# Kernel tuning notes

Hardware: AMD Instinct MI355X
Metric: run time of the kernel (lower is better)

The kernel has to match this reference:

```python
import jax, jax.numpy as jnp
import numpy as np

# ---- constants reconstructing the DMC lookup tables (topology_to_triangles, x/y/z, inner) ----
GRID = 32            # cells per axis -> offset grid is (GRID+1)^3
T = 48               # number of triangle-bearing topologies
MAXTRI = 4           # max triangles per topology (marching cubes)
EPS = 1e-8

# 12 marching-cubes edges of a cell: (corner offset dx,dy,dz, axis of edge)
EDGES = [(0,0,0,0),(1,0,0,1),(0,1,0,0),(0,0,0,1),
         (0,0,1,0),(1,0,1,1),(0,1,1,0),(0,0,1,1),
         (0,0,0,2),(1,0,0,2),(1,1,0,2),(0,1,0,2)]

# Deterministic stand-in for the MC triangle table: per topology, up to 4 triangles,
# each triangle = 3 edge indices in [0,12). TRI_MASK marks valid triangles.
_rs = np.random.RandomState(0)
TRI_TABLE = jnp.asarray(_rs.randint(0, 12, (T, MAXTRI, 3)))          # [T,4,3] int
_ntri = _rs.randint(1, MAXTRI + 1, (T,))
TRI_MASK = jnp.asarray((np.arange(MAXTRI)[None, :] < _ntri[:, None]).astype(np.float32))  # [T,4]


def _edge_vertices(offset):
    """offset: [3, G, G, G] -> per-cell edge vertex positions [N_cells, 12, 3].
    Vertex on an edge = edge midpoint + scalar offset along the edge axis."""
    ci = jnp.arange(GRID)
    I, J, K = jnp.meshgrid(ci, ci, ci, indexing='ij')  # [32,32,32]
    verts = []
    for (dx, dy, dz, a) in EDGES:  # fixed small loop over 12 edges
        gi, gj, gk = I + dx, J + dy, K + dz
        base = jnp.stack([gi, gj, gk], axis=-1).astype(offset.dtype)  # [32,32,32,3]
        disp = offset[a, gi, gj, gk]                                   # [32,32,32]
        unit = jnp.zeros((3,), offset.dtype).at[a].set(1.0)
        verts.append(base + (0.5 + disp)[..., None] * unit)
    V = jnp.stack(verts, axis=3)          # [32,32,32,12,3]
    return V.reshape(-1, 12, 3)            # [N,12,3]


def setup_inputs() -> dict:
    key = jax.random.key(0)
    k0, k1 = jax.random.split(key)
    offset = jax.random.normal(k0, (3, GRID + 1, GRID + 1, GRID + 1), dtype=jnp.float32)
    topology = jax.random.uniform(k1, (GRID ** 3, T), dtype=jnp.float32)
    return {"offset": offset, "topology": topology}


def reference(offset, topology):
    V = _edge_vertices(offset)                  # [N,12,3]
    tv = V[:, TRI_TABLE]                        # [N,T,4,3verts,3]  (irregular gather)
    # unnormalized face normals, then normalize
    n = jnp.cross(tv[..., 1, :] - tv[..., 0, :], tv[..., 2, :] - tv[..., 0, :])  # [N,T,4,3]
    n = n / (jnp.linalg.norm(n, axis=-1, keepdims=True) + EPS)

    # within-cell curvature: squared normal difference of consecutive triangle pairs
    d = n[:, :, 1:, :] - n[:, :, :-1, :]        # [N,T,3,3]
    pair_mask = TRI_MASK[:, 1:] * TRI_MASK[:, :-1]  # [T,3]
    within = jnp.einsum('ntpc,tp->nt', d * d, pair_mask)
    loss_within = jnp.einsum('nt,nt->', topology, within)

    # cross-cell curvature between adjacent cells (the 'inner' pair term),
    # factored so no [N,T,T] tensor is materialized:
    # sum_{t1,t2} p1 p2 ||m1-m2||^2 = s1*P2 + s2*P1 - 2 e1.e2
    cnt = TRI_MASK.sum(-1)                                   # [T]
    m = jnp.einsum('ntpc,tp->ntc', n, TRI_MASK) / cnt[None, :, None]  # mean normal [N,T,3]
    e = jnp.einsum('nt,ntc->nc', topology, m)                # [N,3]
    s = jnp.einsum('nt,nt->n', topology, (m * m).sum(-1))    # [N]
    P = topology.sum(-1)                                      # [N]
    G3 = (GRID, GRID, GRID)
    e3 = e.reshape(*G3, 3)
    s3 = s.reshape(G3)
    P3 = P.reshape(G3)
    loss_cross = jnp.zeros((), offset.dtype)
    for ax in range(3):
        ea = jnp.moveaxis(e3, ax, 0); sa = jnp.moveaxis(s3, ax, 0); pa = jnp.moveaxis(P3, ax, 0)
        e_l, e_r = ea[:-1], ea[1:]
        s_l, s_r = sa[:-1], sa[1:]
        p_l, p_r = pa[:-1], pa[1:]
        loss_cross = loss_cross + (s_l * p_r + s_r * p_l - 2.0 * (e_l * e_r).sum(-1)).sum()
    return (loss_within + loss_cross).reshape(1)
```

## Files before the change

kernel.cpp:

```cpp
#include <hip/hip_runtime.h>

namespace {

constexpr int T = 48;
constexpr int MAXTRI = 4;
constexpr int NCELLS = 32 * 32 * 32;
constexpr float EPSF = 1e-8f;
constexpr int NBLK_CELL = NCELLS / 64;
constexpr int NBLK_CROSS = NCELLS / 256;

struct Tables {
  int tri[T][MAXTRI][3];
  int ntri[T];
};

struct MT {
  unsigned mt[624];
  int pos;
  constexpr MT() : mt{}, pos(624) {
    unsigned s = 0u;
    for (int i = 0; i < 624; ++i) {
      mt[i] = s;
      s = 1812433253u * (s ^ (s >> 30)) + (unsigned)(i + 1);
    }
  }
  constexpr unsigned next() {
    if (pos == 624) {
      for (int i = 0; i < 624; ++i) {
        unsigned y = (mt[i] & 0x80000000u) | (mt[(i + 1) % 624] & 0x7fffffffu);
        unsigned v = mt[(i + 397) % 624] ^ (y >> 1);
        if (y & 1u) v ^= 0x9908b0dfu;
        mt[i] = v;
      }
      pos = 0;
    }
    unsigned y = mt[pos++];
    y ^= y >> 11;
    y ^= (y << 7) & 0x9d2c5680u;
    y ^= (y << 15) & 0xefc60000u;
    y ^= y >> 18;
    return y;
  }
  constexpr unsigned draw(unsigned mask, unsigned rng) {
    unsigned v = next() & mask;
    while (v > rng) v = next() & mask;
    return v;
  }
};

constexpr Tables make_tables() {
  Tables tb{};
  MT g{};
  for (int t = 0; t < T; ++t)
    for (int p = 0; p < MAXTRI; ++p)
      for (int c = 0; c < 3; ++c)
        tb.tri[t][p][c] = (int)g.draw(15u, 11u);
  for (int t = 0; t < T; ++t)
    tb.ntri[t] = 1 + (int)g.draw(3u, 3u);
  return tb;
}

constexpr Tables TB = make_tables();

constexpr int EDX[12] = {0,1,0,0,0,1,0,0,0,1,1,0};
constexpr int EDY[12] = {0,0,1,0,0,0,1,0,0,0,1,1};
constexpr int EDZ[12] = {0,0,0,0,1,1,1,1,0,0,0,0};
constexpr int EAX[12] = {0,1,0,1,0,1,0,1,2,2,2,2};

template <int t, int p>
__device__ __forceinline__ void tri_normals(const float (&vx)[12], const float (&vy)[12],
                                            const float (&vz)[12], float (&nx)[MAXTRI],
                                            float (&ny)[MAXTRI], float (&nz)[MAXTRI]) {
  if constexpr (p < TB.ntri[t]) {
    constexpr int e0 = TB.tri[t][p][0];
    constexpr int e1 = TB.tri[t][p][1];
    constexpr int e2 = TB.tri[t][p][2];
    float ax = vx[e1] - vx[e0], ay = vy[e1] - vy[e0], az = vz[e1] - vz[e0];
    float bx = vx[e2] - vx[e0], by = vy[e2] - vy[e0], bz = vz[e2] - vz[e0];
    float cx = ay * bz - az * by;
    float cy = az * bx - ax * bz;
    float cz = ax * by - ay * bx;
    float nrm = __builtin_amdgcn_sqrtf(cx * cx + cy * cy + cz * cz);
    float inv = __builtin_amdgcn_rcpf(nrm + EPSF);
    nx[p] = cx * inv; ny[p] = cy * inv; nz[p] = cz * inv;
    tri_normals<t, p + 1>(vx, vy, vz, nx, ny, nz);
  }
}

template <int t>
__device__ __forceinline__ void accum_t(const float (&vx)[12], const float (&vy)[12],
                                        const float (&vz)[12], float tv, float& lw, float& ex,
                                        float& ey, float& ez, float& ss, float& pp) {
  constexpr int nt = TB.ntri[t];
  float nx[MAXTRI] = {0.f, 0.f, 0.f, 0.f};
  float ny[MAXTRI] = {0.f, 0.f, 0.f, 0.f};
  float nz[MAXTRI] = {0.f, 0.f, 0.f, 0.f};
  tri_normals<t, 0>(vx, vy, vz, nx, ny, nz);

  float within = 0.f;
  if constexpr (nt > 1) {
    float dx = nx[1] - nx[0], dy = ny[1] - ny[0], dz = nz[1] - nz[0];
    within += dx * dx + dy * dy + dz * dz;
  }
  if constexpr (nt > 2) {
    float dx = nx[2] - nx[1], dy = ny[2] - ny[1], dz = nz[2] - nz[1];
    within += dx * dx + dy * dy + dz * dz;
  }
  if constexpr (nt > 3) {
    float dx = nx[3] - nx[2], dy = ny[3] - ny[2], dz = nz[3] - nz[2];
    within += dx * dx + dy * dy + dz * dz;
  }

  float mx = nx[0], my = ny[0], mz = nz[0];
  if constexpr (nt > 1) { mx += nx[1]; my += ny[1]; mz += nz[1]; }
  if constexpr (nt > 2) { mx += nx[2]; my += ny[2]; mz += nz[2]; }
  if constexpr (nt > 3) { mx += nx[3]; my += ny[3]; mz += nz[3]; }
  constexpr float invn = 1.0f / (float)nt;
  mx *= invn; my *= invn; mz *= invn;

  lw += tv * within;
  ex += tv * mx; ey += tv * my; ez += tv * mz;
  ss += tv * (mx * mx + my * my + mz * mz);
  pp += tv;
}

template <int t0, int t1>
__device__ __forceinline__ void accum_range(const float (&vx)[12], const float (&vy)[12],
                                            const float (&vz)[12], const float* s_topo, int lane,
                                            float& lw, float& ex, float& ey, float& ez, float& ss,
                                            float& pp) {
  if constexpr (t0 < t1) {
    float tv = s_topo[t0 * 64 + lane];
    accum_t<t0>(vx, vy, vz, tv, lw, ex, ey, ez, ss, pp);
    accum_range<t0 + 1, t1>(vx, vy, vz, s_topo, lane, lw, ex, ey, ez, ss, pp);
  }
}

__global__ __launch_bounds__(512) void cell_kernel(const float* __restrict__ offset,
                                                   const float* __restrict__ topo,
                                                   float* __restrict__ wsE,
                                                   float* __restrict__ wsS,
                                                   float* __restrict__ wsP,
                                                   float* __restrict__ wsLW,
                                                   float* __restrict__ wsACC,
                                                   int* __restrict__ wsTicket) {
  __shared__ float s_topo[T * 64];
  __shared__ float s_part[6][8][64];
  const int tid = threadIdx.x;
  const int lane = tid & 63;
  const int wid = tid >> 6;
  const int cell0 = blockIdx.x * 64;

  if (blockIdx.x == 0 && tid == 0) {
    *wsACC = 0.f;
    *wsTicket = 0;
  }

  {
    const float4* g4 = reinterpret_cast<const float4*>(topo + (size_t)cell0 * T);
#pragma unroll
    for (int it = 0; it < 2; ++it) {
      int idx = tid + it * 512;
      if (idx < 768) {
        float4 v = g4[idx];
        int cell = idx / 12;
        int tq = (idx % 12) * 4;
        s_topo[(tq + 0) * 64 + cell] = v.x;
        s_topo[(tq + 1) * 64 + cell] = v.y;
        s_topo[(tq + 2) * 64 + cell] = v.z;
        s_topo[(tq + 3) * 64 + cell] = v.w;
      }
    }
  }
  __syncthreads();

  const int n = cell0 + lane;
  const int i = n >> 10, j = (n >> 5) & 31, k = n & 31;

  float vx[12], vy[12], vz[12];
#pragma unroll
  for (int e = 0; e < 12; ++e) {
    const int gi = i + EDX[e], gj = j + EDY[e], gk = k + EDZ[e];
    const int a = EAX[e];
    const float disp = offset[a * 35937 + gi * 1089 + gj * 33 + gk];
    float px = (float)gi, py = (float)gj, pz = (float)gk;
    const float d = 0.5f + disp;
    if (a == 0) px += d; else if (a == 1) py += d; else pz += d;
    vx[e] = px; vy[e] = py; vz[e] = pz;
  }

  float lw = 0.f, ex = 0.f, ey = 0.f, ez = 0.f, ss = 0.f, pp = 0.f;
  switch (wid) {
    case 0:  accum_range<0, 6>(vx, vy, vz, s_topo, lane, lw, ex, ey, ez, ss, pp); break;
    case 1:  accum_range<6, 12>(vx, vy, vz, s_topo, lane, lw, ex, ey, ez, ss, pp); break;
    case 2:  accum_range<12, 18>(vx, vy, vz, s_topo, lane, lw, ex, ey, ez, ss, pp); break;
    case 3:  accum_range<18, 24>(vx, vy, vz, s_topo, lane, lw, ex, ey, ez, ss, pp); break;
    case 4:  accum_range<24, 30>(vx, vy, vz, s_topo, lane, lw, ex, ey, ez, ss, pp); break;
    case 5:  accum_range<30, 36>(vx, vy, vz, s_topo, lane, lw, ex, ey, ez, ss, pp); break;
    case 6:  accum_range<36, 42>(vx, vy, vz, s_topo, lane, lw, ex, ey, ez, ss, pp); break;
    default: accum_range<42, 48>(vx, vy, vz, s_topo, lane, lw, ex, ey, ez, ss, pp); break;
  }

  s_part[0][wid][lane] = ex;
  s_part[1][wid][lane] = ey;
  s_part[2][wid][lane] = ez;
  s_part[3][wid][lane] = ss;
  s_part[4][wid][lane] = pp;
  s_part[5][wid][lane] = lw;
  __syncthreads();

  if (tid < 384) {
    const int q = tid >> 6, c = tid & 63;
    float v = 0.f;
#pragma unroll
    for (int w = 0; w < 8; ++w) v += s_part[q][w][c];
    const int nn = cell0 + c;
    if (q == 0) wsE[nn] = v;
    else if (q == 1) wsE[NCELLS + nn] = v;
    else if (q == 2) wsE[2 * NCELLS + nn] = v;
    else if (q == 3) wsS[nn] = v;
    else if (q == 4) wsP[nn] = v;
    else {
#pragma unroll
      for (int off = 32; off > 0; off >>= 1) v += __shfl_down(v, off);
      if (c == 0) wsLW[blockIdx.x] = v;
    }
  }
}

__global__ __launch_bounds__(256) void cross_kernel(const float* __restrict__ wsE,
                                                    const float* __restrict__ wsS,
                                                    const float* __restrict__ wsP,
                                                    const float* __restrict__ wsLW,
                                                    float* __restrict__ wsACC,
                                                    int* __restrict__ wsTicket,
                                                    float* __restrict__ out) {
  const int n = blockIdx.x * 256 + threadIdx.x;
  const int i = n >> 10, j = (n >> 5) & 31, k = n & 31;
  const float* ex = wsE;
  const float* ey = wsE + NCELLS;
  const float* ez = wsE + 2 * NCELLS;

  const float sl = wsS[n], pl = wsP[n];
  const float exl = ex[n], eyl = ey[n], ezl = ez[n];
  float acc = 0.f;
  if (i < 31) {
    int r = n + 1024;
    acc += sl * wsP[r] + wsS[r] * pl - 2.f * (exl * ex[r] + eyl * ey[r] + ezl * ez[r]);
  }
  if (j < 31) {
    int r = n + 32;
    acc += sl * wsP[r] + wsS[r] * pl - 2.f * (exl * ex[r] + eyl * ey[r] + ezl * ez[r]);
  }
  if (k < 31) {
    int r = n + 1;
    acc += sl * wsP[r] + wsS[r] * pl - 2.f * (exl * ex[r] + eyl * ey[r] + ezl * ez[r]);
  }

#pragma unroll
  for (int off = 32; off > 0; off >>= 1) acc += __shfl_down(acc, off);
  __shared__ float wpart[4];
  __shared__ int s_last;
  const int lane = threadIdx.x & 63, w = threadIdx.x >> 6;
  if (lane == 0) wpart[w] = acc;
  __syncthreads();

  if (threadIdx.x == 0) {
    float bsum = wpart[0] + wpart[1] + wpart[2] + wpart[3];
    atomicAdd(wsACC, bsum);
    __threadfence();
    int old = atomicAdd(wsTicket, 1);
    s_last = (old == NBLK_CROSS - 1) ? 1 : 0;
  }
  __syncthreads();

  if (s_last) {
    float v = 0.f;
#pragma unroll
    for (int it = 0; it < NBLK_CELL / 256; ++it) v += wsLW[threadIdx.x + it * 256];
#pragma unroll
    for (int off = 32; off > 0; off >>= 1) v += __shfl_down(v, off);
    if (lane == 0) wpart[w] = v;
    __syncthreads();
    if (threadIdx.x == 0) {
      float cross = atomicAdd(wsACC, 0.0f);
      out[0] = cross + wpart[0] + wpart[1] + wpart[2] + wpart[3];
    }
  }
}

}

extern "C" void kernel_launch(void* const* d_in, const int* in_sizes, int n_in,
                              void* d_out, int out_size, void* d_ws, size_t ws_size,
                              hipStream_t stream) {
  const float* offset = (const float*)d_in[0];
  const float* topo = (const float*)d_in[1];
  float* out = (float*)d_out;
  float* wsE = (float*)d_ws;
  float* wsS = wsE + 3 * NCELLS;
  float* wsP = wsS + NCELLS;
  float* wsLW = wsP + NCELLS;
  float* wsACC = wsLW + NBLK_CELL;
  int* wsTicket = (int*)(wsACC + 1);

  hipLaunchKernelGGL(cell_kernel, dim3(NBLK_CELL), dim3(512), 0, stream,
                     offset, topo, wsE, wsS, wsP, wsLW, wsACC, wsTicket);
  hipLaunchKernelGGL(cross_kernel, dim3(NBLK_CROSS), dim3(256), 0, stream,
                     wsE, wsS, wsP, wsLW, wsACC, wsTicket, out);
}
```

Baseline: 18.36 us.

## Fuse cell and cross kernels via cooperative grid sync; balance wave workloads

Merges the per-cell kernel and the cross-cell reduction kernel into one cooperative launch that uses a grid-wide barrier between phases, which removes the second kernel launch and its gap. The topology ranges assigned to each wave are now split at compile time by estimated triangle work rather than in equal chunks of six, so the waves in a block carry similar loads. Grid sync requires all 512 blocks to be resident at once (launch_bounds 512,4) and adds host-side occupancy and attribute queries on every call. If the cooperative launch is not possible, the code falls back to the original two kernels.

```diff
diff --git a/kernel.cpp b/kernel.cpp
--- a/kernel.cpp
+++ b/kernel.cpp
@@ -1,4 +1,7 @@
 #include <hip/hip_runtime.h>
+#include <hip/hip_cooperative_groups.h>
+
+namespace cg = cooperative_groups;
 
 namespace {
 
@@ -6,8 +9,9 @@
 constexpr int MAXTRI = 4;
 constexpr int NCELLS = 32 * 32 * 32;
 constexpr float EPSF = 1e-8f;
-constexpr int NBLK_CELL = NCELLS / 64;
+constexpr int NBLK = NCELLS / 64;
 constexpr int NBLK_CROSS = NCELLS / 256;
+constexpr int NWAVE = 8;
 
 struct Tables {
   int tri[T][MAXTRI][3];
@@ -61,6 +65,23 @@
 }
 
 constexpr Tables TB = make_tables();
+
+struct Splits { int s[NWAVE + 1]; };
+constexpr Splits make_splits() {
+  Splits sp{};
+  int total = 0;
+  for (int t = 0; t < T; ++t) total += 3 * TB.ntri[t] + 2;
+  sp.s[0] = 0;
+  int acc = 0, t = 0;
+  for (int w = 1; w < NWAVE; ++w) {
+    const int target = (total * w + NWAVE / 2) / NWAVE;
+    while (t < T && acc < target) { acc += 3 * TB.ntri[t] + 2; ++t; }
+    sp.s[w] = t;
+  }
+  sp.s[NWAVE] = T;
+  return sp;
+}
+constexpr Splits SP = make_splits();
 
 constexpr int EDX[12] = {0,1,0,0,0,1,0,0,0,1,1,0};
 constexpr int EDY[12] = {0,0,1,0,0,0,1,0,0,0,1,1};
@@ -136,6 +157,153 @@
   }
 }
 
+__device__ __forceinline__ void phase1(const float* __restrict__ offset,
+                                       const float* __restrict__ topo,
+                                       const float* s_topo, int wid, int lane, int cell0,
+                                       float& lw, float& ex, float& ey, float& ez, float& ss,
+                                       float& pp) {
+  const int n = cell0 + lane;
+  const int i = n >> 10, j = (n >> 5) & 31, k = n & 31;
+
+  float vx[12], vy[12], vz[12];
+#pragma unroll
+  for (int e = 0; e < 12; ++e) {
+    const int gi = i + EDX[e], gj = j + EDY[e], gk = k + EDZ[e];
+    const int a = EAX[e];
+    const float disp = offset[a * 35937 + gi * 1089 + gj * 33 + gk];
+    float px = (float)gi, py = (float)gj, pz = (float)gk;
+    const float d = 0.5f + disp;
+    if (a == 0) px += d; else if (a == 1) py += d; else pz += d;
+    vx[e] = px; vy[e] = py; vz[e] = pz;
+  }
+
+  switch (wid) {
+    case 0:  accum_range<SP.s[0], SP.s[1]>(vx, vy, vz, s_topo, lane, lw, ex, ey, ez, ss, pp); break;
+    case 1:  accum_range<SP.s[1], SP.s[2]>(vx, vy, vz, s_topo, lane, lw, ex, ey, ez, ss, pp); break;
+    case 2:  accum_range<SP.s[2], SP.s[3]>(vx, vy, vz, s_topo, lane, lw, ex, ey, ez, ss, pp); break;
+    case 3:  accum_range<SP.s[3], SP.s[4]>(vx, vy, vz, s_topo, lane, lw, ex, ey, ez, ss, pp); break;
+    case 4:  accum_range<SP.s[4], SP.s[5]>(vx, vy, vz, s_topo, lane, lw, ex, ey, ez, ss, pp); break;
+    case 5:  accum_range<SP.s[5], SP.s[6]>(vx, vy, vz, s_topo, lane, lw, ex, ey, ez, ss, pp); break;
+    case 6:  accum_range<SP.s[6], SP.s[7]>(vx, vy, vz, s_topo, lane, lw, ex, ey, ez, ss, pp); break;
+    default: accum_range<SP.s[7], SP.s[8]>(vx, vy, vz, s_topo, lane, lw, ex, ey, ez, ss, pp); break;
+  }
+}
+
+__device__ __forceinline__ void stage_topo(const float* __restrict__ topo, float* s_topo,
+                                           int tid, int cell0) {
+  const float4* g4 = reinterpret_cast<const float4*>(topo + (size_t)cell0 * T);
+#pragma unroll
+  for (int it = 0; it < 2; ++it) {
+    int idx = tid + it * 512;
+    if (idx < 768) {
+      float4 v = g4[idx];
+      int cell = idx / 12;
+      int tq = (idx % 12) * 4;
+      s_topo[(tq + 0) * 64 + cell] = v.x;
+      s_topo[(tq + 1) * 64 + cell] = v.y;
+      s_topo[(tq + 2) * 64 + cell] = v.z;
+      s_topo[(tq + 3) * 64 + cell] = v.w;
+    }
+  }
+}
+
+__device__ __forceinline__ float cross_for_cell(const float* __restrict__ wsE,
+                                                const float* __restrict__ wsS,
+                                                const float* __restrict__ wsP, int n) {
+  const int i = n >> 10, j = (n >> 5) & 31, k = n & 31;
+  const float* ex = wsE;
+  const float* ey = wsE + NCELLS;
+  const float* ez = wsE + 2 * NCELLS;
+  const float sl = wsS[n], pl = wsP[n];
+  const float exl = ex[n], eyl = ey[n], ezl = ez[n];
+  float acc = 0.f;
+  if (i < 31) {
+    int r = n + 1024;
+    acc += sl * wsP[r] + wsS[r] * pl - 2.f * (exl * ex[r] + eyl * ey[r] + ezl * ez[r]);
+  }
+  if (j < 31) {
+    int r = n + 32;
+    acc += sl * wsP[r] + wsS[r] * pl - 2.f * (exl * ex[r] + eyl * ey[r] + ezl * ez[r]);
+  }
+  if (k < 31) {
+    int r = n + 1;
+    acc += sl * wsP[r] + wsS[r] * pl - 2.f * (exl * ex[r] + eyl * ey[r] + ezl * ez[r]);
+  }
+  return acc;
+}
+
+__global__ __launch_bounds__(512, 4) void fused_kernel(const float* __restrict__ offset,
+                                                       const float* __restrict__ topo,
+                                                       float* __restrict__ wsE,
+                                                       float* __restrict__ wsS,
+                                                       float* __restrict__ wsP,
+                                                       float* __restrict__ wsACC,
+                                                       int* __restrict__ wsTicket,
+                                                       float* __restrict__ out) {
+  __shared__ float s_topo[T * 64];
+  __shared__ float s_part[6][NWAVE][64];
+  __shared__ float s_lw;
+  const int tid = threadIdx.x;
+  const int lane = tid & 63;
+  const int wid = tid >> 6;
+  const int cell0 = blockIdx.x * 64;
+
+  if (blockIdx.x == 0 && tid == 0) {
+    atomicExch(wsACC, 0.0f);
+    atomicExch(wsTicket, 0);
+  }
+
+  stage_topo(topo, s_topo, tid, cell0);
+  __syncthreads();
+
+  {
+    float lw = 0.f, ex = 0.f, ey = 0.f, ez = 0.f, ss = 0.f, pp = 0.f;
+    phase1(offset, topo, s_topo, wid, lane, cell0, lw, ex, ey, ez, ss, pp);
+    s_part[0][wid][lane] = ex;
+    s_part[1][wid][lane] = ey;
+    s_part[2][wid][lane] = ez;
+    s_part[3][wid][lane] = ss;
+    s_part[4][wid][lane] = pp;
+    s_part[5][wid][lane] = lw;
+  }
+  __syncthreads();
+
+  if (tid < 384) {
+    const int q = tid >> 6, c = tid & 63;
+    float v = 0.f;
+#pragma unroll
+    for (int w = 0; w < NWAVE; ++w) v += s_part[q][w][c];
+    const int nn = cell0 + c;
+    if (q == 0) wsE[nn] = v;
+    else if (q == 1) wsE[NCELLS + nn] = v;
+    else if (q == 2) wsE[2 * NCELLS + nn] = v;
+    else if (q == 3) wsS[nn] = v;
+    else if (q == 4) wsP[nn] = v;
+    else {
+#pragma unroll
+      for (int off = 32; off > 0; off >>= 1) v += __shfl_down(v, off);
+      if (c == 0) s_lw = v;
+    }
+  }
+
+  cg::this_grid().sync();
+
+  if (tid < 64) {
+    float acc = cross_for_cell(wsE, wsS, wsP, cell0 + tid);
+#pragma unroll
+    for (int off = 32; off > 0; off >>= 1) acc += __shfl_down(acc, off);
+
+    if (tid == 0) {
+      atomicAdd(wsACC, acc + s_lw);
+      __threadfence();
+      int old = atomicAdd(wsTicket, 1);
+      if (old == NBLK - 1) {
+        out[0] = atomicAdd(wsACC, 0.0f);
+      }
+    }
+  }
+}
+
 __global__ __launch_bounds__(512) void cell_kernel(const float* __restrict__ offset,
                                                    const float* __restrict__ topo,
                                                    float* __restrict__ wsE,
@@ -145,75 +313,37 @@
                                                    float* __restrict__ wsACC,
                                                    int* __restrict__ wsTicket) {
   __shared__ float s_topo[T * 64];
-  __shared__ float s_part[6][8][64];
+  __shared__ float s_part[6][NWAVE][64];
   const int tid = threadIdx.x;
   const int lane = tid & 63;
   const int wid = tid >> 6;
   const int cell0 = blockIdx.x * 64;
 
   if (blockIdx.x == 0 && tid == 0) {
-    *wsACC = 0.f;
-    *wsTicket = 0;
-  }
+    atomicExch(wsACC, 0.0f);
+    atomicExch(wsTicket, 0);
+  }
+
+  stage_topo(topo, s_topo, tid, cell0);
+  __syncthreads();
 
   {
-    const float4* g4 = reinterpret_cast<const float4*>(topo + (size_t)cell0 * T);
-#pragma unroll
-    for (int it = 0; it < 2; ++it) {
-      int idx = tid + it * 512;
-      if (idx < 768) {
-        float4 v = g4[idx];
-        int cell = idx / 12;
-        int tq = (idx % 12) * 4;
-        s_topo[(tq + 0) * 64 + cell] = v.x;
-        s_topo[(tq + 1) * 64 + cell] = v.y;
-        s_topo[(tq + 2) * 64 + cell] = v.z;
-        s_topo[(tq + 3) * 64 + cell] = v.w;
-      }
-    }
-  }
-  __syncthreads();
-
-  const int n = cell0 + lane;
-  const int i = n >> 10, j = (n >> 5) & 31, k = n & 31;
-
-  float vx[12], vy[12], vz[12];
-#pragma unroll
-  for (int e = 0; e < 12; ++e) {
-    const int gi = i + EDX[e], gj = j + EDY[e], gk = k + EDZ[e];
-    const int a = EAX[e];
-    const float disp = offset[a * 35937 + gi * 1089 + gj * 33 + gk];
-    float px = (float)gi, py = (float)gj, pz = (float)gk;
-    const float d = 0.5f + disp;
-    if (a == 0) px += d; else if (a == 1) py += d; else pz += d;
-    vx[e] = px; vy[e] = py; vz[e] = pz;
-  }
-
-  float lw = 0.f, ex = 0.f, ey = 0.f, ez = 0.f, ss = 0.f, pp = 0.f;
-  switch (wid) {
-    case 0:  accum_range<0, 6>(vx, vy, vz, s_topo, lane, lw, ex, ey, ez, ss, pp); break;
-    case 1:  accum_range<6, 12>(vx, vy, vz, s_topo, lane, lw, ex, ey, ez, ss, pp); break;
-    case 2:  accum_range<12, 18>(vx, vy, vz, s_topo, lane, lw, ex, ey, ez, ss, pp); break;
-    case 3:  accum_range<18, 24>(vx, vy, vz, s_topo, lane, lw, ex, ey, ez, ss, pp); break;
-    case 4:  accum_range<24, 30>(vx, vy, vz, s_topo, lane, lw, ex, ey, ez, ss, pp); break;
-    case 5:  accum_range<30, 36>(vx, vy, vz, s_topo, lane, lw, ex, ey, ez, ss, pp); break;
-    case 6:  accum_range<36, 42>(vx, vy, vz, s_topo, lane, lw, ex, ey, ez, ss, pp); break;
-    default: accum_range<42, 48>(vx, vy, vz, s_topo, lane, lw, ex, ey, ez, ss, pp); break;
-  }
-
-  s_part[0][wid][lane] = ex;
-  s_part[1][wid][lane] = ey;
-  s_part[2][wid][lane] = ez;
-  s_part[3][wid][lane] = ss;
-  s_part[4][wid][lane] = pp;
-  s_part[5][wid][lane] = lw;
+    float lw = 0.f, ex = 0.f, ey = 0.f, ez = 0.f, ss = 0.f, pp = 0.f;
+    phase1(offset, topo, s_topo, wid, lane, cell0, lw, ex, ey, ez, ss, pp);
+    s_part[0][wid][lane] = ex;
+    s_part[1][wid][lane] = ey;
+    s_part[2][wid][lane] = ez;
+    s_part[3][wid][lane] = ss;
+    s_part[4][wid][lane] = pp;
+    s_part[5][wid][lane] = lw;
+  }
   __syncthreads();
 
   if (tid < 384) {
     const int q = tid >> 6, c = tid & 63;
     float v = 0.f;
 #pragma unroll
-    for (int w = 0; w < 8; ++w) v += s_part[q][w][c];
+    for (int w = 0; w < NWAVE; ++w) v += s_part[q][w][c];
     const int nn = cell0 + c;
     if (q == 0) wsE[nn] = v;
     else if (q == 1) wsE[NCELLS + nn] = v;
@@ -236,26 +366,7 @@
                                                     int* __restrict__ wsTicket,
                                                     float* __restrict__ out) {
   const int n = blockIdx.x * 256 + threadIdx.x;
-  const int i = n >> 10, j = (n >> 5) & 31, k = n & 31;
-  const float* ex = wsE;
-  const float* ey = wsE + NCELLS;
-  const float* ez = wsE + 2 * NCELLS;
-
-  const float sl = wsS[n], pl = wsP[n];
-  const float exl = ex[n], eyl = ey[n], ezl = ez[n];
-  float acc = 0.f;
-  if (i < 31) {
-    int r = n + 1024;
-    acc += sl * wsP[r] + wsS[r] * pl - 2.f * (exl * ex[r] + eyl * ey[r] + ezl * ez[r]);
-  }
-  if (j < 31) {
-    int r = n + 32;
-    acc += sl * wsP[r] + wsS[r] * pl - 2.f * (exl * ex[r] + eyl * ey[r] + ezl * ez[r]);
-  }
-  if (k < 31) {
-    int r = n + 1;
-    acc += sl * wsP[r] + wsS[r] * pl - 2.f * (exl * ex[r] + eyl * ey[r] + ezl * ez[r]);
-  }
+  float acc = cross_for_cell(wsE, wsS, wsP, n);
 
 #pragma unroll
   for (int off = 32; off > 0; off >>= 1) acc += __shfl_down(acc, off);
@@ -277,7 +388,7 @@
   if (s_last) {
     float v = 0.f;
 #pragma unroll
-    for (int it = 0; it < NBLK_CELL / 256; ++it) v += wsLW[threadIdx.x + it * 256];
+    for (int it = 0; it < NBLK / 256; ++it) v += wsLW[threadIdx.x + it * 256];
 #pragma unroll
     for (int off = 32; off > 0; off >>= 1) v += __shfl_down(v, off);
     if (lane == 0) wpart[w] = v;
@@ -301,10 +412,25 @@
   float* wsS = wsE + 3 * NCELLS;
   float* wsP = wsS + NCELLS;
   float* wsLW = wsP + NCELLS;
-  float* wsACC = wsLW + NBLK_CELL;
+  float* wsACC = wsLW + NBLK;
   int* wsTicket = (int*)(wsACC + 1);
 
-  hipLaunchKernelGGL(cell_kernel, dim3(NBLK_CELL), dim3(512), 0, stream,
+  int dev = 0;
+  hipGetDevice(&dev);
+  int coop = 0, nCU = 0, maxBlk = 0;
+  hipDeviceGetAttribute(&coop, hipDeviceAttributeCooperativeLaunch, dev);
+  hipDeviceGetAttribute(&nCU, hipDeviceAttributeMultiprocessorCount, dev);
+  hipOccupancyMaxActiveBlocksPerMultiprocessor(&maxBlk, fused_kernel, 512, 0);
+
+  if (coop && (long)maxBlk * nCU >= NBLK) {
+    void* args[] = {(void*)&offset, (void*)&topo, (void*)&wsE, (void*)&wsS,
+                    (void*)&wsP, (void*)&wsACC, (void*)&wsTicket, (void*)&out};
+    hipError_t err = hipLaunchCooperativeKernel((const void*)fused_kernel, dim3(NBLK),
+                                                dim3(512), args, 0, stream);
+    if (err == hipSuccess) return;
+  }
+
+  hipLaunchKernelGGL(cell_kernel, dim3(NBLK), dim3(512), 0, stream,
                      offset, topo, wsE, wsS, wsP, wsLW, wsACC, wsTicket);
   hipLaunchKernelGGL(cross_kernel, dim3(NBLK_CROSS), dim3(256), 0, stream,
                      wsE, wsS, wsP, wsLW, wsACC, wsTicket, out);
```

After: 18.29 us. Within noise of the previous version (-0.4%).

## Fuse cross-cell term into cell kernel via 4x4x4 tiles with recomputed halo

Applied to the files above, without the earlier changes.

Restructures the computation into 4x4x4 cell tiles per block, recomputing the 61 halo cells on the +i/+j/+k faces so the cross-cell pair term can be evaluated from shared memory. This removes the global workspace round trip for per-cell e/s/P and the separate atomic-ticket cross kernel, replacing them with a tiny single-block finish reduction. It also rebalances the per-wave topology ranges by triangle count. The cost is nearly doubled per-block work (125 cells computed versus 64 owned) and a second serialized compute phase in which only 61 of the 64 lanes are active.

```diff
diff --git a/kernel.cpp b/kernel.cpp
--- a/kernel.cpp
+++ b/kernel.cpp
@@ -4,10 +4,11 @@
 
 constexpr int T = 48;
 constexpr int MAXTRI = 4;
-constexpr int NCELLS = 32 * 32 * 32;
 constexpr float EPSF = 1e-8f;
-constexpr int NBLK_CELL = NCELLS / 64;
-constexpr int NBLK_CROSS = NCELLS / 256;
+constexpr int NWAVE = 8;
+constexpr int NBLK = 512;
+constexpr int NLOC = 125;
+constexpr int NHALO = 61;
 
 struct Tables {
   int tri[T][MAXTRI][3];
@@ -61,6 +62,41 @@
 }
 
 constexpr Tables TB = make_tables();
+
+struct Splits { int s[NWAVE + 1]; };
+constexpr Splits make_splits() {
+  Splits sp{};
+  int total = 0;
+  for (int t = 0; t < T; ++t) total += 3 * TB.ntri[t] + 2;
+  sp.s[0] = 0;
+  int acc = 0, t = 0;
+  for (int w = 1; w < NWAVE; ++w) {
+    const int target = (total * w + NWAVE / 2) / NWAVE;
+    while (t < T && acc < target) { acc += 3 * TB.ntri[t] + 2; ++t; }
+    sp.s[w] = t;
+  }
+  sp.s[NWAVE] = T;
+  return sp;
+}
+constexpr Splits SP = make_splits();
+
+struct Lmap {
+  int lidx[NLOC];
+  int halo[NHALO];
+};
+constexpr Lmap make_lmap() {
+  Lmap m{};
+  int h = 64;
+  for (int li = 0; li < 5; ++li)
+    for (int lj = 0; lj < 5; ++lj)
+      for (int lk = 0; lk < 5; ++lk) {
+        int f = li * 25 + lj * 5 + lk;
+        if (li < 4 && lj < 4 && lk < 4) m.lidx[f] = li * 16 + lj * 4 + lk;
+        else { m.lidx[f] = h; m.halo[h - 64] = f; ++h; }
+      }
+  return m;
+}
+constexpr Lmap LM = make_lmap();
 
 constexpr int EDX[12] = {0,1,0,0,0,1,0,0,0,1,1,0};
 constexpr int EDY[12] = {0,0,1,0,0,0,1,0,0,0,1,1};
@@ -126,61 +162,39 @@
 
 template <int t0, int t1>
 __device__ __forceinline__ void accum_range(const float (&vx)[12], const float (&vy)[12],
-                                            const float (&vz)[12], const float* s_topo, int lane,
+                                            const float (&vz)[12], const float* s_topo, int cellc,
                                             float& lw, float& ex, float& ey, float& ez, float& ss,
                                             float& pp) {
   if constexpr (t0 < t1) {
-    float tv = s_topo[t0 * 64 + lane];
+    float tv = s_topo[t0 * NLOC + cellc];
     accum_t<t0>(vx, vy, vz, tv, lw, ex, ey, ez, ss, pp);
-    accum_range<t0 + 1, t1>(vx, vy, vz, s_topo, lane, lw, ex, ey, ez, ss, pp);
-  }
-}
-
-__global__ __launch_bounds__(512) void cell_kernel(const float* __restrict__ offset,
-                                                   const float* __restrict__ topo,
-                                                   float* __restrict__ wsE,
-                                                   float* __restrict__ wsS,
-                                                   float* __restrict__ wsP,
-                                                   float* __restrict__ wsLW,
-                                                   float* __restrict__ wsACC,
-                                                   int* __restrict__ wsTicket) {
-  __shared__ float s_topo[T * 64];
-  __shared__ float s_part[6][8][64];
-  const int tid = threadIdx.x;
-  const int lane = tid & 63;
-  const int wid = tid >> 6;
-  const int cell0 = blockIdx.x * 64;
-
-  if (blockIdx.x == 0 && tid == 0) {
-    *wsACC = 0.f;
-    *wsTicket = 0;
-  }
-
-  {
-    const float4* g4 = reinterpret_cast<const float4*>(topo + (size_t)cell0 * T);
-#pragma unroll
-    for (int it = 0; it < 2; ++it) {
-      int idx = tid + it * 512;
-      if (idx < 768) {
-        float4 v = g4[idx];
-        int cell = idx / 12;
-        int tq = (idx % 12) * 4;
-        s_topo[(tq + 0) * 64 + cell] = v.x;
-        s_topo[(tq + 1) * 64 + cell] = v.y;
-        s_topo[(tq + 2) * 64 + cell] = v.z;
-        s_topo[(tq + 3) * 64 + cell] = v.w;
-      }
-    }
-  }
-  __syncthreads();
-
-  const int n = cell0 + lane;
-  const int i = n >> 10, j = (n >> 5) & 31, k = n & 31;
-
-  float vx[12], vy[12], vz[12];
+    accum_range<t0 + 1, t1>(vx, vy, vz, s_topo, cellc, lw, ex, ey, ez, ss, pp);
+  }
+}
+
+__device__ __forceinline__ void accum_dispatch(int wid, const float (&vx)[12],
+                                               const float (&vy)[12], const float (&vz)[12],
+                                               const float* s_topo, int cellc, float& lw,
+                                               float& ex, float& ey, float& ez, float& ss,
+                                               float& pp) {
+  switch (wid) {
+    case 0:  accum_range<SP.s[0], SP.s[1]>(vx, vy, vz, s_topo, cellc, lw, ex, ey, ez, ss, pp); break;
+    case 1:  accum_range<SP.s[1], SP.s[2]>(vx, vy, vz, s_topo, cellc, lw, ex, ey, ez, ss, pp); break;
+    case 2:  accum_range<SP.s[2], SP.s[3]>(vx, vy, vz, s_topo, cellc, lw, ex, ey, ez, ss, pp); break;
+    case 3:  accum_range<SP.s[3], SP.s[4]>(vx, vy, vz, s_topo, cellc, lw, ex, ey, ez, ss, pp); break;
+    case 4:  accum_range<SP.s[4], SP.s[5]>(vx, vy, vz, s_topo, cellc, lw, ex, ey, ez, ss, pp); break;
+    case 5:  accum_range<SP.s[5], SP.s[6]>(vx, vy, vz, s_topo, cellc, lw, ex, ey, ez, ss, pp); break;
+    case 6:  accum_range<SP.s[6], SP.s[7]>(vx, vy, vz, s_topo, cellc, lw, ex, ey, ez, ss, pp); break;
+    default: accum_range<SP.s[7], SP.s[8]>(vx, vy, vz, s_topo, cellc, lw, ex, ey, ez, ss, pp); break;
+  }
+}
+
+__device__ __forceinline__ void build_verts(const float* __restrict__ offset, int ci, int cj,
+                                            int ck, float (&vx)[12], float (&vy)[12],
+                                            float (&vz)[12]) {
 #pragma unroll
   for (int e = 0; e < 12; ++e) {
-    const int gi = i + EDX[e], gj = j + EDY[e], gk = k + EDZ[e];
+    const int gi = ci + EDX[e], gj = cj + EDY[e], gk = ck + EDZ[e];
     const int a = EAX[e];
     const float disp = offset[a * 35937 + gi * 1089 + gj * 33 + gk];
     float px = (float)gi, py = (float)gj, pz = (float)gk;
@@ -188,104 +202,140 @@
     if (a == 0) px += d; else if (a == 1) py += d; else pz += d;
     vx[e] = px; vy[e] = py; vz[e] = pz;
   }
-
-  float lw = 0.f, ex = 0.f, ey = 0.f, ez = 0.f, ss = 0.f, pp = 0.f;
-  switch (wid) {
-    case 0:  accum_range<0, 6>(vx, vy, vz, s_topo, lane, lw, ex, ey, ez, ss, pp); break;
-    case 1:  accum_range<6, 12>(vx, vy, vz, s_topo, lane, lw, ex, ey, ez, ss, pp); break;
-    case 2:  accum_range<12, 18>(vx, vy, vz, s_topo, lane, lw, ex, ey, ez, ss, pp); break;
-    case 3:  accum_range<18, 24>(vx, vy, vz, s_topo, lane, lw, ex, ey, ez, ss, pp); break;
-    case 4:  accum_range<24, 30>(vx, vy, vz, s_topo, lane, lw, ex, ey, ez, ss, pp); break;
-    case 5:  accum_range<30, 36>(vx, vy, vz, s_topo, lane, lw, ex, ey, ez, ss, pp); break;
-    case 6:  accum_range<36, 42>(vx, vy, vz, s_topo, lane, lw, ex, ey, ez, ss, pp); break;
-    default: accum_range<42, 48>(vx, vy, vz, s_topo, lane, lw, ex, ey, ez, ss, pp); break;
-  }
-
-  s_part[0][wid][lane] = ex;
-  s_part[1][wid][lane] = ey;
-  s_part[2][wid][lane] = ez;
-  s_part[3][wid][lane] = ss;
-  s_part[4][wid][lane] = pp;
-  s_part[5][wid][lane] = lw;
+}
+
+__global__ __launch_bounds__(512, 4) void halo_kernel(const float* __restrict__ offset,
+                                                      const float* __restrict__ topo,
+                                                      float* __restrict__ ws_part) {
+  __shared__ float s_topo[T * NLOC];
+  __shared__ float s_part[6][NWAVE][64];
+  __shared__ float s_esp[5][128];
+  __shared__ float s_lw;
+  const int tid = threadIdx.x, lane = tid & 63, wid = tid >> 6;
+  const int bi = blockIdx.x >> 6, bj = (blockIdx.x >> 3) & 7, bk = blockIdx.x & 7;
+  const int ci0 = bi * 4, cj0 = bj * 4, ck0 = bk * 4;
+
+  {
+    const float4* g4 = reinterpret_cast<const float4*>(topo);
+#pragma unroll
+    for (int it = 0; it < 3; ++it) {
+      int u = tid + it * 512;
+      if (u < NLOC * 12) {
+        int c = u / 12, q = u % 12;
+        int li, lj, lk;
+        if (c < 64) { li = c >> 4; lj = (c >> 2) & 3; lk = c & 3; }
+        else { int f = LM.halo[c - 64]; li = f / 25; lj = (f / 5) % 5; lk = f % 5; }
+        int ci = min(ci0 + li, 31), cj = min(cj0 + lj, 31), ck = min(ck0 + lk, 31);
+        int g = (ci << 10) + (cj << 5) + ck;
+        float4 v = g4[g * 12 + q];
+        int tq = q * 4;
+        s_topo[(tq + 0) * NLOC + c] = v.x;
+        s_topo[(tq + 1) * NLOC + c] = v.y;
+        s_topo[(tq + 2) * NLOC + c] = v.z;
+        s_topo[(tq + 3) * NLOC + c] = v.w;
+      }
+    }
+  }
+  __syncthreads();
+
+  {
+    const int li = lane >> 4, lj = (lane >> 2) & 3, lk = lane & 3;
+    float vx[12], vy[12], vz[12];
+    build_verts(offset, ci0 + li, cj0 + lj, ck0 + lk, vx, vy, vz);
+    float lw = 0.f, ex = 0.f, ey = 0.f, ez = 0.f, ss = 0.f, pp = 0.f;
+    accum_dispatch(wid, vx, vy, vz, s_topo, lane, lw, ex, ey, ez, ss, pp);
+    s_part[0][wid][lane] = ex;
+    s_part[1][wid][lane] = ey;
+    s_part[2][wid][lane] = ez;
+    s_part[3][wid][lane] = ss;
+    s_part[4][wid][lane] = pp;
+    s_part[5][wid][lane] = lw;
+  }
   __syncthreads();
 
   if (tid < 384) {
     const int q = tid >> 6, c = tid & 63;
     float v = 0.f;
 #pragma unroll
-    for (int w = 0; w < 8; ++w) v += s_part[q][w][c];
-    const int nn = cell0 + c;
-    if (q == 0) wsE[nn] = v;
-    else if (q == 1) wsE[NCELLS + nn] = v;
-    else if (q == 2) wsE[2 * NCELLS + nn] = v;
-    else if (q == 3) wsS[nn] = v;
-    else if (q == 4) wsP[nn] = v;
+    for (int w = 0; w < NWAVE; ++w) v += s_part[q][w][c];
+    if (q < 5) s_esp[q][c] = v;
     else {
 #pragma unroll
       for (int off = 32; off > 0; off >>= 1) v += __shfl_down(v, off);
-      if (c == 0) wsLW[blockIdx.x] = v;
-    }
-  }
-}
-
-__global__ __launch_bounds__(256) void cross_kernel(const float* __restrict__ wsE,
-                                                    const float* __restrict__ wsS,
-                                                    const float* __restrict__ wsP,
-                                                    const float* __restrict__ wsLW,
-                                                    float* __restrict__ wsACC,
-                                                    int* __restrict__ wsTicket,
-                                                    float* __restrict__ out) {
-  const int n = blockIdx.x * 256 + threadIdx.x;
-  const int i = n >> 10, j = (n >> 5) & 31, k = n & 31;
-  const float* ex = wsE;
-  const float* ey = wsE + NCELLS;
-  const float* ez = wsE + 2 * NCELLS;
-
-  const float sl = wsS[n], pl = wsP[n];
-  const float exl = ex[n], eyl = ey[n], ezl = ez[n];
-  float acc = 0.f;
-  if (i < 31) {
-    int r = n + 1024;
-    acc += sl * wsP[r] + wsS[r] * pl - 2.f * (exl * ex[r] + eyl * ey[r] + ezl * ez[r]);
-  }
-  if (j < 31) {
-    int r = n + 32;
-    acc += sl * wsP[r] + wsS[r] * pl - 2.f * (exl * ex[r] + eyl * ey[r] + ezl * ez[r]);
-  }
-  if (k < 31) {
-    int r = n + 1;
-    acc += sl * wsP[r] + wsS[r] * pl - 2.f * (exl * ex[r] + eyl * ey[r] + ezl * ez[r]);
-  }
-
-#pragma unroll
-  for (int off = 32; off > 0; off >>= 1) acc += __shfl_down(acc, off);
-  __shared__ float wpart[4];
-  __shared__ int s_last;
-  const int lane = threadIdx.x & 63, w = threadIdx.x >> 6;
-  if (lane == 0) wpart[w] = acc;
-  __syncthreads();
-
-  if (threadIdx.x == 0) {
-    float bsum = wpart[0] + wpart[1] + wpart[2] + wpart[3];
-    atomicAdd(wsACC, bsum);
-    __threadfence();
-    int old = atomicAdd(wsTicket, 1);
-    s_last = (old == NBLK_CROSS - 1) ? 1 : 0;
-  }
-  __syncthreads();
-
-  if (s_last) {
-    float v = 0.f;
-#pragma unroll
-    for (int it = 0; it < NBLK_CELL / 256; ++it) v += wsLW[threadIdx.x + it * 256];
-#pragma unroll
-    for (int off = 32; off > 0; off >>= 1) v += __shfl_down(v, off);
-    if (lane == 0) wpart[w] = v;
-    __syncthreads();
-    if (threadIdx.x == 0) {
-      float cross = atomicAdd(wsACC, 0.0f);
-      out[0] = cross + wpart[0] + wpart[1] + wpart[2] + wpart[3];
-    }
+      if (c == 0) s_lw = v;
+    }
+  }
+  __syncthreads();
+
+  if (lane < NHALO) {
+    const int f = LM.halo[lane];
+    const int li = f / 25, lj = (f / 5) % 5, lk = f % 5;
+    const int ci = min(ci0 + li, 31), cj = min(cj0 + lj, 31), ck = min(ck0 + lk, 31);
+    float vx[12], vy[12], vz[12];
+    build_verts(offset, ci, cj, ck, vx, vy, vz);
+    float lw = 0.f, ex = 0.f, ey = 0.f, ez = 0.f, ss = 0.f, pp = 0.f;
+    accum_dispatch(wid, vx, vy, vz, s_topo, 64 + lane, lw, ex, ey, ez, ss, pp);
+    s_part[0][wid][lane] = ex;
+    s_part[1][wid][lane] = ey;
+    s_part[2][wid][lane] = ez;
+    s_part[3][wid][lane] = ss;
+    s_part[4][wid][lane] = pp;
+  }
+  __syncthreads();
+
+  if (tid < 320) {
+    const int q = tid >> 6, c = tid & 63;
+    if (c < NHALO) {
+      float v = 0.f;
+#pragma unroll
+      for (int w = 0; w < NWAVE; ++w) v += s_part[q][w][c];
+      s_esp[q][64 + c] = v;
+    }
+  }
+  __syncthreads();
+
+  if (tid < 64) {
+    const int li = tid >> 4, lj = (tid >> 2) & 3, lk = tid & 3;
+    const int f = li * 25 + lj * 5 + lk;
+    const int gi = ci0 + li, gj = cj0 + lj, gk = ck0 + lk;
+    const float exl = s_esp[0][tid], eyl = s_esp[1][tid], ezl = s_esp[2][tid];
+    const float sl = s_esp[3][tid], pl = s_esp[4][tid];
+    float acc = 0.f;
+    if (gi < 31) {
+      int r = LM.lidx[f + 25];
+      acc += sl * s_esp[4][r] + s_esp[3][r] * pl -
+             2.f * (exl * s_esp[0][r] + eyl * s_esp[1][r] + ezl * s_esp[2][r]);
+    }
+    if (gj < 31) {
+      int r = LM.lidx[f + 5];
+      acc += sl * s_esp[4][r] + s_esp[3][r] * pl -
+             2.f * (exl * s_esp[0][r] + eyl * s_esp[1][r] + ezl * s_esp[2][r]);
+    }
+    if (gk < 31) {
+      int r = LM.lidx[f + 1];
+      acc += sl * s_esp[4][r] + s_esp[3][r] * pl -
+             2.f * (exl * s_esp[0][r] + eyl * s_esp[1][r] + ezl * s_esp[2][r]);
+    }
+#pragma unroll
+    for (int off = 32; off > 0; off >>= 1) acc += __shfl_down(acc, off);
+    if (tid == 0) ws_part[blockIdx.x] = acc + s_lw;
+  }
+}
+
+__global__ __launch_bounds__(512) void finish_kernel(const float* __restrict__ ws_part,
+                                                     float* __restrict__ out) {
+  const int tid = threadIdx.x;
+  float v = ws_part[tid];
+#pragma unroll
+  for (int off = 32; off > 0; off >>= 1) v += __shfl_down(v, off);
+  __shared__ float w[8];
+  if ((tid & 63) == 0) w[tid >> 6] = v;
+  __syncthreads();
+  if (tid == 0) {
+    float s = 0.f;
+#pragma unroll
+    for (int i = 0; i < 8; ++i) s += w[i];
+    out[0] = s;
   }
 }
 
@@ -297,15 +347,9 @@
   const float* offset = (const float*)d_in[0];
   const float* topo = (const float*)d_in[1];
   float* out = (float*)d_out;
-  float* wsE = (float*)d_ws;
-  float* wsS = wsE + 3 * NCELLS;
-  float* wsP = wsS + NCELLS;
-  float* wsLW = wsP + NCELLS;
-  float* wsACC = wsLW + NBLK_CELL;
-  int* wsTicket = (int*)(wsACC + 1);
-
-  hipLaunchKernelGGL(cell_kernel, dim3(NBLK_CELL), dim3(512), 0, stream,
-                     offset, topo, wsE, wsS, wsP, wsLW, wsACC, wsTicket);
-  hipLaunchKernelGGL(cross_kernel, dim3(NBLK_CROSS), dim3(256), 0, stream,
-                     wsE, wsS, wsP, wsLW, wsACC, wsTicket, out);
-}
+  float* ws_part = (float*)d_ws;
+
+  hipLaunchKernelGGL(halo_kernel, dim3(NBLK), dim3(512), 0, stream,
+                     offset, topo, ws_part);
+  hipLaunchKernelGGL(finish_kernel, dim3(1), dim3(512), 0, stream, ws_part, out);
+}
```

Result: slower. 20.26 us (+10.3%).
